# Kernel optimization log

Hardware: AMD Instinct MI355X
Metric: run time of the kernel (lower is better)

## Reference

```python
import jax, jax.numpy as jnp
import numpy as np

B, T_Q, T_KV, D = 4, 2048, 4096, 1024
H = 16
HD = D // H  # head_dim = 64
EPS_LN = 1e-5
EPS_NORM = 1e-12


def setup_inputs() -> dict:
    key = jax.random.key(0)
    ks = jax.random.split(key, 12)
    inp = {
        'query': jax.random.normal(ks[0], (B, T_Q, D), jnp.float32),
        'key':   jax.random.normal(ks[1], (B, T_KV, D), jnp.float32),
        'value': jax.random.normal(ks[2], (B, T_KV, D), jnp.float32),
        # projections (nn.Linear stores weight as [out, in]; y = x @ W.T)
        'Wq': jax.random.normal(ks[3], (D, D), jnp.float32) * 0.02,
        'Wk': jax.random.normal(ks[4], (D, D), jnp.float32) * 0.02,
        'Wv': jax.random.normal(ks[5], (D, D), jnp.float32) * 0.02,
        'Wo': jax.random.normal(ks[6], (D, D), jnp.float32) * 0.01,
        'bo': jnp.zeros((D,), jnp.float32),
        'Wbeta':  jax.random.normal(ks[7], (H, D), jnp.float32) * 0.02,
        'bbeta':  jnp.zeros((H,), jnp.float32),
        'Walpha': jax.random.normal(ks[8], (H, D), jnp.float32) * 0.02,
        'balpha': jnp.full((H,), -1.0, jnp.float32),
        # per-head-dim LayerNorms
        'gq': jnp.ones((HD,), jnp.float32),
        'bq': jnp.zeros((HD,), jnp.float32),
        'gk': jnp.ones((HD,), jnp.float32),
        'bk': jnp.zeros((HD,), jnp.float32),
    }
    return inp


def _layernorm(x, g, b):
    mu = jnp.mean(x, axis=-1, keepdims=True)
    var = jnp.mean(jnp.square(x - mu), axis=-1, keepdims=True)
    return (x - mu) * jax.lax.rsqrt(var + EPS_LN) * g + b


def reference(query, key, value, Wq, Wk, Wv, Wo, bo,
              Wbeta, bbeta, Walpha, balpha, gq, bq, gk, bk):
    Bq, Tq, Dm = query.shape
    Tkv = key.shape[1]

    q = (query @ Wq.T).reshape(Bq, Tq, H, HD)
    k = (key   @ Wk.T).reshape(Bq, Tkv, H, HD)
    v = (value @ Wv.T).reshape(Bq, Tkv, H, HD)

    q = _layernorm(q, gq, bq)
    k = _layernorm(k, gk, bk)
    # F.normalize(k, dim=-1)
    k = k / jnp.maximum(jnp.linalg.norm(k, axis=-1, keepdims=True), EPS_NORM)

    beta  = jax.nn.sigmoid(key @ Wbeta.T  + bbeta)   # [B, Tkv, H]
    alpha = jax.nn.sigmoid(key @ Walpha.T + balpha)  # [B, Tkv, H]

    # time-major for scan: [Tkv, B, H, ...]
    k_t = jnp.moveaxis(k, 1, 0)
    v_t = jnp.moveaxis(v, 1, 0)
    b_t = jnp.moveaxis(beta, 1, 0)
    a_t = jnp.moveaxis(alpha, 1, 0)

    M0 = jnp.zeros((Bq, H, HD, HD), query.dtype)

    def step(M, inputs):
        kt, vt, bt, at = inputs  # [B,H,d],[B,H,d],[B,H],[B,H]
        Mk = jnp.einsum('bhij,bhj->bhi', M, kt)
        erase = at[..., None, None] * jnp.einsum('bhi,bhj->bhij', Mk, kt)
        write = bt[..., None, None] * jnp.einsum('bhi,bhj->bhij', vt, kt)
        return M - erase + write, None

    M, _ = jax.lax.scan(step, M0, (k_t, v_t, b_t, a_t))

    # out[b,t,h,i] = sum_j M[b,h,i,j] * q[b,t,h,j]
    out = jnp.einsum('bhij,bthj->bthi', M, q).reshape(Bq, Tq, Dm)
    out = out @ Wo.T + bo  # dropout is identity in eval mode
    return out
```

## Files before the change

### kernel.cpp

```cpp
#include <hip/hip_runtime.h>
#include <math.h>

#define TQ_LEN 2048
#define TKV_LEN 4096
#define BATCH 4
#define DMODEL 1024
#define NH 16
#define HD 64
#define NKBA 1152
#define CCH 128
#define NCHUNK (TKV_LEN / CCH)

typedef unsigned short u16;
typedef __attribute__((ext_vector_type(8))) short bf16x8;
typedef __attribute__((ext_vector_type(4))) float f32x4;

__device__ __forceinline__ u16 f2bf(float x) {
  union { float f; unsigned u; } c; c.f = x;
  unsigned r = c.u + 0x7fffu + ((c.u >> 16) & 1u);
  return (u16)(r >> 16);
}
__device__ __forceinline__ float bf2f(u16 x) {
  union { unsigned u; float f; } c; c.u = ((unsigned)x) << 16;
  return c.f;
}

__device__ __forceinline__ float wave_sum64(float x) {
#pragma unroll
  for (int off = 32; off; off >>= 1) x += __shfl_xor(x, off, 64);
  return x;
}

__global__ __launch_bounds__(256) void cvt_bf16_kernel(
    const float* __restrict__ s, u16* __restrict__ d) {
  size_t i = ((size_t)blockIdx.x * 256 + threadIdx.x) * 8;
  float4 a = *(const float4*)&s[i];
  float4 b = *(const float4*)&s[i + 4];
  union { u16 h[8]; uint4 v; } o;
  o.h[0] = f2bf(a.x); o.h[1] = f2bf(a.y); o.h[2] = f2bf(a.z); o.h[3] = f2bf(a.w);
  o.h[4] = f2bf(b.x); o.h[5] = f2bf(b.y); o.h[6] = f2bf(b.z); o.h[7] = f2bf(b.w);
  *(uint4*)&d[i] = o.v;
}

__global__ __launch_bounds__(256) void wcat_bf_kernel(
    const float* __restrict__ Wk, const float* __restrict__ Wb,
    const float* __restrict__ Wa, u16* __restrict__ Wcat) {
  int i = blockIdx.x * 256 + threadIdx.x;
  int row = i / DMODEL, col = i % DMODEL;
  float v;
  if (row < 1024)      v = Wk[i];
  else if (row < 1040) v = Wb[(row - 1024) * DMODEL + col];
  else if (row < 1056) v = Wa[(row - 1040) * DMODEL + col];
  else                 v = 0.f;
  Wcat[i] = f2bf(v);
}

__device__ __forceinline__ void stage_tile_bf16(
    const u16* __restrict__ G, int ldg, int row0, int kcol0,
    u16* lds, int wid, int lane) {
#pragma unroll
  for (int e = 0; e < 2; ++e) {
    int r = (wid * 2 + e) * 16;
    const u16* g = G + (size_t)(row0 + r + (lane >> 2)) * ldg + kcol0 + (lane & 3) * 8;
    __builtin_amdgcn_global_load_lds(
        (const __attribute__((address_space(1))) void*)g,
        (__attribute__((address_space(3))) void*)(lds + r * 32), 16, 0, 0);
  }
}

template <bool HAS_BIAS, bool OUT_BF16>
__global__ __launch_bounds__(256) void gemm_bt_bf16(
    const u16* __restrict__ A, const u16* __restrict__ B,
    const float* __restrict__ bias, void* __restrict__ Cv,
    int M, int N, int K, int ldc, int nbx) {
  __shared__ u16 Al[2][128 * 32];
  __shared__ u16 Bl[2][128 * 32];
  const int tid = threadIdx.x;
  const int wid = tid >> 6, lane = tid & 63;
  const int wr = wid >> 1, wc = wid & 1;
  const int nwg = gridDim.x;
  const int cpx = nwg >> 3;
  const int orig = blockIdx.x;
  const int swz = (orig & 7) * cpx + (orig >> 3);
  const int bm = (swz / nbx) * 128, bn = (swz % nbx) * 128;
  const int lrow = lane & 15, lk = (lane >> 4) * 8;

  int aoff[4], boff[4];
#pragma unroll
  for (int f = 0; f < 4; ++f) {
    aoff[f] = (wr * 64 + f * 16 + lrow) * 32 + lk;
    boff[f] = (wc * 64 + f * 16 + lrow) * 32 + lk;
  }

  f32x4 acc[4][4] = {};
  const int nk = K >> 5;
  int cur = 0;
  stage_tile_bf16(A, K, bm, 0, &Al[0][0], wid, lane);
  stage_tile_bf16(B, K, bn, 0, &Bl[0][0], wid, lane);
  __syncthreads();
  for (int kt = 0; kt < nk; ++kt) {
    if (kt + 1 < nk) {
      stage_tile_bf16(A, K, bm, (kt + 1) * 32, &Al[cur ^ 1][0], wid, lane);
      stage_tile_bf16(B, K, bn, (kt + 1) * 32, &Bl[cur ^ 1][0], wid, lane);
    }
    bf16x8 af[4], bfr[4];
#pragma unroll
    for (int f = 0; f < 4; ++f) af[f] = *(const bf16x8*)&Al[cur][aoff[f]];
#pragma unroll
    for (int f = 0; f < 4; ++f) bfr[f] = *(const bf16x8*)&Bl[cur][boff[f]];
#pragma unroll
    for (int mf = 0; mf < 4; ++mf)
#pragma unroll
      for (int nf = 0; nf < 4; ++nf)
        acc[mf][nf] = __builtin_amdgcn_mfma_f32_16x16x32_bf16(
            af[mf], bfr[nf], acc[mf][nf], 0, 0, 0);
    __syncthreads();
    cur ^= 1;
  }
  const int crow0 = bm + wr * 64 + (lane >> 4) * 4;
  const int ccol0 = bn + wc * 64 + (lane & 15);
#pragma unroll
  for (int mf = 0; mf < 4; ++mf)
#pragma unroll
    for (int nf = 0; nf < 4; ++nf) {
      int col = ccol0 + nf * 16;
      float bv = HAS_BIAS ? bias[col] : 0.f;
#pragma unroll
      for (int i = 0; i < 4; ++i) {
        int row = crow0 + mf * 16 + i;
        float vout = acc[mf][nf][i] + bv;
        if (OUT_BF16)
          ((u16*)Cv)[(size_t)row * ldc + col] = f2bf(vout);
        else
          ((float*)Cv)[(size_t)row * ldc + col] = vout;
      }
    }
}

__global__ __launch_bounds__(256) void ln_q_kernel(float* __restrict__ q,
                                                   const float* __restrict__ g,
                                                   const float* __restrict__ b) {
  int gidx = blockIdx.x * 4 + (threadIdx.x >> 6);
  int lane = threadIdx.x & 63;
  int row = gidx >> 4, h = gidx & 15;
  float* p = q + (size_t)row * DMODEL + h * HD + lane;
  float x = *p;
  float mu = wave_sum64(x) * (1.f / 64.f);
  float d = x - mu;
  float var = wave_sum64(d * d) * (1.f / 64.f);
  float y = d * rsqrtf(var + 1e-5f) * g[lane] + b[lane];
  *p = y;
}

__global__ __launch_bounds__(256) void ln_k_kernel(float* __restrict__ kb,
                                                   const float* __restrict__ g,
                                                   const float* __restrict__ b) {
  int gidx = blockIdx.x * 4 + (threadIdx.x >> 6);
  int lane = threadIdx.x & 63;
  int row = gidx >> 4, h = gidx & 15;
  float* p = kb + (size_t)row * NKBA + h * HD + lane;
  float x = *p;
  float mu = wave_sum64(x) * (1.f / 64.f);
  float d = x - mu;
  float var = wave_sum64(d * d) * (1.f / 64.f);
  float y = d * rsqrtf(var + 1e-5f) * g[lane] + b[lane];
  float s2 = wave_sum64(y * y);
  y = y / fmaxf(sqrtf(s2), 1e-12f);
  *p = y;
}

__global__ __launch_bounds__(256) void sig_kernel(
    const float* __restrict__ kb, const float* __restrict__ bb,
    const float* __restrict__ ba, float* __restrict__ beta,
    float* __restrict__ alpha) {
  int i = blockIdx.x * 256 + threadIdx.x;
  int row = i >> 4, h = i & 15;
  float lb = kb[(size_t)row * NKBA + 1024 + h] + bb[h];
  float la = kb[(size_t)row * NKBA + 1040 + h] + ba[h];
  beta[i]  = 1.f / (1.f + expf(-lb));
  alpha[i] = 1.f / (1.f + expf(-la));
}

__global__ __launch_bounds__(64, 2) void chunk_scan_kernel(
    const float* __restrict__ kb, const u16* __restrict__ v,
    const float* __restrict__ beta, const float* __restrict__ alpha,
    float* __restrict__ Pbuf, float* __restrict__ Sbuf) {
  __shared__ float klds[2][64];
  int slot = blockIdx.x;
  int bh = slot / NCHUNK, ck = slot % NCHUNK;
  int b = bh >> 4, h = bh & 15;
  int lane = threadIdx.x;
  int t0 = ck * CCH;
  const float* kbase = kb + ((size_t)b * TKV_LEN + t0) * NKBA + h * HD;
  const u16* vbase = v + ((size_t)b * TKV_LEN + t0) * DMODEL + h * HD;
  const float* bbase = beta + ((size_t)b * TKV_LEN + t0) * NH + h;
  const float* abase = alpha + ((size_t)b * TKV_LEN + t0) * NH + h;

  float P[64], S[64];
#pragma unroll
  for (int j = 0; j < 64; ++j) { P[j] = (j == lane) ? 1.f : 0.f; S[j] = 0.f; }

  klds[0][lane] = kbase[lane];
  float kn = kbase[(size_t)NKBA + lane];
  float vn = bf2f(vbase[lane]);
  float btn = bbase[0];
  float atn = abase[0];

  for (int t = 0; t < CCH; ++t) {
    float vc = vn, bt = btn, at = atn;
    if (t + 1 < CCH) {
      vn = bf2f(vbase[(size_t)(t + 1) * DMODEL + lane]);
      btn = bbase[(size_t)(t + 1) * NH];
      atn = abase[(size_t)(t + 1) * NH];
    }
    klds[(t + 1) & 1][lane] = kn;
    kn = (t + 2 < CCH) ? kbase[(size_t)(t + 2) * NKBA + lane] : 0.f;
    const float* kcur = klds[t & 1];
    float pk0 = 0.f, pk1 = 0.f, sk0 = 0.f, sk1 = 0.f;
#pragma unroll
    for (int g = 0; g < 4; ++g) {
      float4 ka = *(const float4*)&kcur[g * 16 + 0];
      float4 kc = *(const float4*)&kcur[g * 16 + 4];
      float4 ke = *(const float4*)&kcur[g * 16 + 8];
      float4 kg = *(const float4*)&kcur[g * 16 + 12];
      pk0 = fmaf(P[g*16+ 0], ka.x, pk0); pk1 = fmaf(P[g*16+ 1], ka.y, pk1);
      pk0 = fmaf(P[g*16+ 2], ka.z, pk0); pk1 = fmaf(P[g*16+ 3], ka.w, pk1);
      pk0 = fmaf(P[g*16+ 4], kc.x, pk0); pk1 = fmaf(P[g*16+ 5], kc.y, pk1);
      pk0 = fmaf(P[g*16+ 6], kc.z, pk0); pk1 = fmaf(P[g*16+ 7], kc.w, pk1);
      pk0 = fmaf(P[g*16+ 8], ke.x, pk0); pk1 = fmaf(P[g*16+ 9], ke.y, pk1);
      pk0 = fmaf(P[g*16+10], ke.z, pk0); pk1 = fmaf(P[g*16+11], ke.w, pk1);
      pk0 = fmaf(P[g*16+12], kg.x, pk0); pk1 = fmaf(P[g*16+13], kg.y, pk1);
      pk0 = fmaf(P[g*16+14], kg.z, pk0); pk1 = fmaf(P[g*16+15], kg.w, pk1);
      sk0 = fmaf(S[g*16+ 0], ka.x, sk0); sk1 = fmaf(S[g*16+ 1], ka.y, sk1);
      sk0 = fmaf(S[g*16+ 2], ka.z, sk0); sk1 = fmaf(S[g*16+ 3], ka.w, sk1);
      sk0 = fmaf(S[g*16+ 4], kc.x, sk0); sk1 = fmaf(S[g*16+ 5], kc.y, sk1);
      sk0 = fmaf(S[g*16+ 6], kc.z, sk0); sk1 = fmaf(S[g*16+ 7], kc.w, sk1);
      sk0 = fmaf(S[g*16+ 8], ke.x, sk0); sk1 = fmaf(S[g*16+ 9], ke.y, sk1);
      sk0 = fmaf(S[g*16+10], ke.z, sk0); sk1 = fmaf(S[g*16+11], ke.w, sk1);
      sk0 = fmaf(S[g*16+12], kg.x, sk0); sk1 = fmaf(S[g*16+13], kg.y, sk1);
      sk0 = fmaf(S[g*16+14], kg.z, sk0); sk1 = fmaf(S[g*16+15], kg.w, sk1);
    }
    float cp = -at * (pk0 + pk1);
    float cs = fmaf(bt, vc, -at * (sk0 + sk1));
#pragma unroll
    for (int g = 0; g < 4; ++g) {
      float4 ka = *(const float4*)&kcur[g * 16 + 0];
      float4 kc = *(const float4*)&kcur[g * 16 + 4];
      float4 ke = *(const float4*)&kcur[g * 16 + 8];
      float4 kg = *(const float4*)&kcur[g * 16 + 12];
      P[g*16+ 0] = fmaf(cp, ka.x, P[g*16+ 0]); P[g*16+ 1] = fmaf(cp, ka.y, P[g*16+ 1]);
      P[g*16+ 2] = fmaf(cp, ka.z, P[g*16+ 2]); P[g*16+ 3] = fmaf(cp, ka.w, P[g*16+ 3]);
      P[g*16+ 4] = fmaf(cp, kc.x, P[g*16+ 4]); P[g*16+ 5] = fmaf(cp, kc.y, P[g*16+ 5]);
      P[g*16+ 6] = fmaf(cp, kc.z, P[g*16+ 6]); P[g*16+ 7] = fmaf(cp, kc.w, P[g*16+ 7]);
      P[g*16+ 8] = fmaf(cp, ke.x, P[g*16+ 8]); P[g*16+ 9] = fmaf(cp, ke.y, P[g*16+ 9]);
      P[g*16+10] = fmaf(cp, ke.z, P[g*16+10]); P[g*16+11] = fmaf(cp, ke.w, P[g*16+11]);
      P[g*16+12] = fmaf(cp, kg.x, P[g*16+12]); P[g*16+13] = fmaf(cp, kg.y, P[g*16+13]);
      P[g*16+14] = fmaf(cp, kg.z, P[g*16+14]); P[g*16+15] = fmaf(cp, kg.w, P[g*16+15]);
      S[g*16+ 0] = fmaf(cs, ka.x, S[g*16+ 0]); S[g*16+ 1] = fmaf(cs, ka.y, S[g*16+ 1]);
      S[g*16+ 2] = fmaf(cs, ka.z, S[g*16+ 2]); S[g*16+ 3] = fmaf(cs, ka.w, S[g*16+ 3]);
      S[g*16+ 4] = fmaf(cs, kc.x, S[g*16+ 4]); S[g*16+ 5] = fmaf(cs, kc.y, S[g*16+ 5]);
      S[g*16+ 6] = fmaf(cs, kc.z, S[g*16+ 6]); S[g*16+ 7] = fmaf(cs, kc.w, S[g*16+ 7]);
      S[g*16+ 8] = fmaf(cs, ke.x, S[g*16+ 8]); S[g*16+ 9] = fmaf(cs, ke.y, S[g*16+ 9]);
      S[g*16+10] = fmaf(cs, ke.z, S[g*16+10]); S[g*16+11] = fmaf(cs, ke.w, S[g*16+11]);
      S[g*16+12] = fmaf(cs, kg.x, S[g*16+12]); S[g*16+13] = fmaf(cs, kg.y, S[g*16+13]);
      S[g*16+14] = fmaf(cs, kg.z, S[g*16+14]); S[g*16+15] = fmaf(cs, kg.w, S[g*16+15]);
    }
  }
  float* po = Pbuf + (size_t)slot * 4096 + (size_t)lane * 64;
  float* so = Sbuf + (size_t)slot * 4096 + (size_t)lane * 64;
#pragma unroll
  for (int j4 = 0; j4 < 16; ++j4) {
    *(float4*)&po[j4 * 4] = make_float4(P[4 * j4], P[4 * j4 + 1], P[4 * j4 + 2], P[4 * j4 + 3]);
    *(float4*)&so[j4 * 4] = make_float4(S[4 * j4], S[4 * j4 + 1], S[4 * j4 + 2], S[4 * j4 + 3]);
  }
}

__global__ __launch_bounds__(256) void fold_kernel(
    const float* __restrict__ Pin, const float* __restrict__ Sin,
    float* __restrict__ Pout, float* __restrict__ Sout, int nitems) {
  __shared__ float Pa[64][68], Sa[64][68], Pc[64][68], Sc[64][68];
  const int tid = threadIdx.x;
  const int r0 = (tid >> 4) * 4, c0 = (tid & 15) * 4;
  for (int l = tid; l < 4096; l += 256) {
    int r = l >> 6, c = l & 63;
    Pa[r][c] = (r == c) ? 1.f : 0.f;
    Sa[r][c] = 0.f;
  }
  for (int item = 0; item < nitems; ++item) {
    const float* pg = Pin + ((size_t)blockIdx.x * nitems + item) * 4096;
    const float* sg = Sin + ((size_t)blockIdx.x * nitems + item) * 4096;
#pragma unroll
    for (int e = 0; e < 4; ++e) {
      int l = tid * 16 + e * 4;
      int r = l >> 6, c = l & 63;
      *(float4*)&Pc[r][c] = *(const float4*)&pg[l];
      *(float4*)&Sc[r][c] = *(const float4*)&sg[l];
    }
    __syncthreads();
    float accP[4][4] = {}, accS[4][4] = {};
#pragma unroll 4
    for (int j4 = 0; j4 < 16; ++j4) {
      float bmat[4][4];
#pragma unroll
      for (int jj = 0; jj < 4; ++jj) {
        float4 t = *(const float4*)&Pc[j4 * 4 + jj][c0];
        bmat[jj][0] = t.x; bmat[jj][1] = t.y; bmat[jj][2] = t.z; bmat[jj][3] = t.w;
      }
#pragma unroll
      for (int rr = 0; rr < 4; ++rr) {
        float4 tp = *(const float4*)&Pa[r0 + rr][j4 * 4];
        float4 ts = *(const float4*)&Sa[r0 + rr][j4 * 4];
        float ap[4] = {tp.x, tp.y, tp.z, tp.w};
        float as[4] = {ts.x, ts.y, ts.z, ts.w};
#pragma unroll
        for (int jj = 0; jj < 4; ++jj)
#pragma unroll
          for (int cc = 0; cc < 4; ++cc) {
            accP[rr][cc] = fmaf(ap[jj], bmat[jj][cc], accP[rr][cc]);
            accS[rr][cc] = fmaf(as[jj], bmat[jj][cc], accS[rr][cc]);
          }
      }
    }
#pragma unroll
    for (int rr = 0; rr < 4; ++rr)
#pragma unroll
      for (int cc = 0; cc < 4; ++cc) accS[rr][cc] += Sc[r0 + rr][c0 + cc];
    __syncthreads();
#pragma unroll
    for (int rr = 0; rr < 4; ++rr)
#pragma unroll
      for (int cc = 0; cc < 4; ++cc) {
        Pa[r0 + rr][c0 + cc] = accP[rr][cc];
        Sa[r0 + rr][c0 + cc] = accS[rr][cc];
      }
  }
  __syncthreads();
  float* po = Pout + (size_t)blockIdx.x * 4096;
  float* so = Sout + (size_t)blockIdx.x * 4096;
#pragma unroll
  for (int e = 0; e < 4; ++e) {
    int l = tid * 16 + e * 4;
    int r = l >> 6, c = l & 63;
    *(float4*)&po[l] = *(const float4*)&Pa[r][c];
    *(float4*)&so[l] = *(const float4*)&Sa[r][c];
  }
}

__global__ __launch_bounds__(256) void outm_kernel(
    const float* __restrict__ Mg, const float* __restrict__ q,
    u16* __restrict__ attn) {
  __shared__ float Ml[64][65];
  int bh = blockIdx.x;
  int tchunk = blockIdx.y;
  int b = bh >> 4, h = bh & 15;
  int tid = threadIdx.x;
  const float* mg = Mg + (size_t)bh * 4096;
#pragma unroll
  for (int e = 0; e < 16; ++e) {
    int l = tid + e * 256;
    Ml[l >> 6][l & 63] = mg[l];
  }
  __syncthreads();
  int lane = tid & 63, tt = tid >> 6;
  const float* qb = q + ((size_t)b * TQ_LEN + tchunk * 256) * DMODEL + h * HD;
  u16* ob = attn + ((size_t)b * TQ_LEN + tchunk * 256) * DMODEL + h * HD;
  for (int it = 0; it < 64; ++it) {
    int t = it * 4 + tt;
    const float* qr = qb + (size_t)t * DMODEL;
    float acc = 0.f;
#pragma unroll
    for (int j4 = 0; j4 < 16; ++j4) {
      float4 qv = *(const float4*)&qr[j4 * 4];
      acc += Ml[lane][j4 * 4 + 0] * qv.x + Ml[lane][j4 * 4 + 1] * qv.y +
             Ml[lane][j4 * 4 + 2] * qv.z + Ml[lane][j4 * 4 + 3] * qv.w;
    }
    ob[(size_t)t * DMODEL + lane] = f2bf(acc);
  }
}

extern "C" void kernel_launch(void* const* d_in, const int* in_sizes, int n_in,
                              void* d_out, int out_size, void* d_ws,
                              size_t ws_size, hipStream_t stream) {
  const float* query = (const float*)d_in[0];
  const float* key   = (const float*)d_in[1];
  const float* value = (const float*)d_in[2];
  const float* Wq    = (const float*)d_in[3];
  const float* Wk    = (const float*)d_in[4];
  const float* Wv    = (const float*)d_in[5];
  const float* Wo    = (const float*)d_in[6];
  const float* bo    = (const float*)d_in[7];
  const float* Wbeta = (const float*)d_in[8];
  const float* bbeta = (const float*)d_in[9];
  const float* Walpha= (const float*)d_in[10];
  const float* balpha= (const float*)d_in[11];
  const float* gq    = (const float*)d_in[12];
  const float* bq    = (const float*)d_in[13];
  const float* gk    = (const float*)d_in[14];
  const float* bk    = (const float*)d_in[15];
  float* out = (float*)d_out;

  const int MQ = BATCH * TQ_LEN;
  const int MKV = BATCH * TKV_LEN;
  const int NSLOT = 64 * NCHUNK;

  float* ws = (float*)d_ws;
  size_t off = 0;
  u16* Wcat_bf = (u16*)(ws + off); off += (size_t)NKBA * DMODEL / 2;
  u16* Wq_bf   = (u16*)(ws + off); off += (size_t)DMODEL * DMODEL / 2;
  u16* Wv_bf   = (u16*)(ws + off); off += (size_t)DMODEL * DMODEL / 2;
  u16* Wo_bf   = (u16*)(ws + off); off += (size_t)DMODEL * DMODEL / 2;
  u16* qbf = (u16*)(ws + off); size_t qbf_f = off; off += (size_t)MQ * DMODEL / 2;
  u16* kbf = (u16*)(ws + off); size_t kbf_f = off; off += (size_t)MKV * DMODEL / 2;
  u16* vbf = (u16*)(ws + off); size_t vbf_f = off; off += (size_t)MKV * DMODEL / 2;
  float* qp   = ws + off; off += (size_t)MQ * DMODEL;
  float* kba  = ws + off; size_t kba_f = off; off += (size_t)MKV * NKBA;
  u16* vpb = (u16*)(ws + off); off += (size_t)MKV * DMODEL / 2;
  float* Pbuf = ws + kbf_f;
  float* Sbuf = ws + vbf_f;
  float* Gp   = ws + qbf_f;
  float* Gs   = ws + qbf_f + 1048576;
  float* Fp   = ws + qbf_f + 2097152;
  float* beta = ws + qbf_f + 2359296;
  float* alpha= ws + qbf_f + 2621440;
  float* Mg   = ws + qbf_f + 2883584;
  u16* attn_bf = (u16*)(ws + kba_f);

  wcat_bf_kernel<<<NKBA * DMODEL / 256, 256, 0, stream>>>(Wk, Wbeta, Walpha, Wcat_bf);
  cvt_bf16_kernel<<<DMODEL * DMODEL / 2048, 256, 0, stream>>>(Wq, Wq_bf);
  cvt_bf16_kernel<<<DMODEL * DMODEL / 2048, 256, 0, stream>>>(Wv, Wv_bf);
  cvt_bf16_kernel<<<DMODEL * DMODEL / 2048, 256, 0, stream>>>(Wo, Wo_bf);
  cvt_bf16_kernel<<<MQ * DMODEL / 2048, 256, 0, stream>>>(query, qbf);
  cvt_bf16_kernel<<<MKV * DMODEL / 2048, 256, 0, stream>>>(key, kbf);
  cvt_bf16_kernel<<<MKV * DMODEL / 2048, 256, 0, stream>>>(value, vbf);
  gemm_bt_bf16<false, false><<<(DMODEL / 128) * (MQ / 128), 256, 0, stream>>>(
      qbf, Wq_bf, nullptr, qp, MQ, DMODEL, DMODEL, DMODEL, DMODEL / 128);
  gemm_bt_bf16<false, false><<<(NKBA / 128) * (MKV / 128), 256, 0, stream>>>(
      kbf, Wcat_bf, nullptr, kba, MKV, NKBA, DMODEL, NKBA, NKBA / 128);
  gemm_bt_bf16<false, true><<<(DMODEL / 128) * (MKV / 128), 256, 0, stream>>>(
      vbf, Wv_bf, nullptr, vpb, MKV, DMODEL, DMODEL, DMODEL, DMODEL / 128);
  ln_q_kernel<<<MQ * NH / 4, 256, 0, stream>>>(qp, gq, bq);
  ln_k_kernel<<<MKV * NH / 4, 256, 0, stream>>>(kba, gk, bk);
  sig_kernel<<<MKV * NH / 256, 256, 0, stream>>>(kba, bbeta, balpha, beta, alpha);
  chunk_scan_kernel<<<NSLOT, 64, 0, stream>>>(kba, vpb, beta, alpha, Pbuf, Sbuf);
  fold_kernel<<<NSLOT / 8, 256, 0, stream>>>(Pbuf, Sbuf, Gp, Gs, 8);
  fold_kernel<<<64, 256, 0, stream>>>(Gp, Gs, Fp, Mg, 4);
  outm_kernel<<<dim3(64, TQ_LEN / 256), 256, 0, stream>>>(Mg, qp, attn_bf);
  gemm_bt_bf16<true, false><<<(DMODEL / 128) * (MQ / 128), 256, 0, stream>>>(
      attn_bf, Wo_bf, bo, out, MQ, DMODEL, DMODEL, DMODEL, DMODEL / 128);
  (void)in_sizes; (void)n_in; (void)out_size; (void)ws_size;
}
```

Before: 584.2 us.

## Co-schedule Q projection GEMM with chunk scan in one heterogeneous launch

Merges the Q projection GEMM and the per-chunk delta-rule scan into a single kernel: the first blocks run scan work with four waves each, and the remaining blocks run the 128x128 MFMA GEMM tile for Q. The aim is to fill idle compute units during the latency-bound scan with independent GEMM work, removing one serialized launch. Beta and alpha move to fresh workspace so they do not alias buffers the fused kernel writes, and ln_q runs after the fused kernel. The scan blocks now pack four waves under launch_bounds 256, which changes register and occupancy behaviour of the register-heavy scan and may cause spilling or lower occupancy.

```diff
diff --git a/kernel.cpp b/kernel.cpp
--- a/kernel.cpp
+++ b/kernel.cpp
@@ -137,6 +137,165 @@
     }
 }
 
+__global__ __launch_bounds__(256) void fused_qgemm_scan_kernel(
+    const u16* __restrict__ qbf, const u16* __restrict__ Wq_bf,
+    float* __restrict__ qp,
+    const float* __restrict__ kb, const u16* __restrict__ v,
+    const float* __restrict__ beta, const float* __restrict__ alpha,
+    float* __restrict__ Pbuf, float* __restrict__ Sbuf, int nscan) {
+  __shared__ u16 Al[2][128 * 32];
+  __shared__ u16 Bl[2][128 * 32];
+  __shared__ float klds[4][2][64];
+
+  if ((int)blockIdx.x >= nscan) {
+    const int tid = threadIdx.x;
+    const int wid = tid >> 6, lane = tid & 63;
+    const int wr = wid >> 1, wc = wid & 1;
+    const int nwg = gridDim.x - nscan;
+    const int cpx = nwg >> 3;
+    const int orig = (int)blockIdx.x - nscan;
+    const int swz = (orig & 7) * cpx + (orig >> 3);
+    const int nbx = DMODEL / 128;
+    const int bm = (swz / nbx) * 128, bn = (swz % nbx) * 128;
+    const int lrow = lane & 15, lk = (lane >> 4) * 8;
+
+    int aoff[4], boff[4];
+#pragma unroll
+    for (int f = 0; f < 4; ++f) {
+      aoff[f] = (wr * 64 + f * 16 + lrow) * 32 + lk;
+      boff[f] = (wc * 64 + f * 16 + lrow) * 32 + lk;
+    }
+
+    f32x4 acc[4][4] = {};
+    const int nk = DMODEL >> 5;
+    int cur = 0;
+    stage_tile_bf16(qbf, DMODEL, bm, 0, &Al[0][0], wid, lane);
+    stage_tile_bf16(Wq_bf, DMODEL, bn, 0, &Bl[0][0], wid, lane);
+    __syncthreads();
+    for (int kt = 0; kt < nk; ++kt) {
+      if (kt + 1 < nk) {
+        stage_tile_bf16(qbf, DMODEL, bm, (kt + 1) * 32, &Al[cur ^ 1][0], wid, lane);
+        stage_tile_bf16(Wq_bf, DMODEL, bn, (kt + 1) * 32, &Bl[cur ^ 1][0], wid, lane);
+      }
+      bf16x8 af[4], bfr[4];
+#pragma unroll
+      for (int f = 0; f < 4; ++f) af[f] = *(const bf16x8*)&Al[cur][aoff[f]];
+#pragma unroll
+      for (int f = 0; f < 4; ++f) bfr[f] = *(const bf16x8*)&Bl[cur][boff[f]];
+#pragma unroll
+      for (int mf = 0; mf < 4; ++mf)
+#pragma unroll
+        for (int nf = 0; nf < 4; ++nf)
+          acc[mf][nf] = __builtin_amdgcn_mfma_f32_16x16x32_bf16(
+              af[mf], bfr[nf], acc[mf][nf], 0, 0, 0);
+      __syncthreads();
+      cur ^= 1;
+    }
+    const int crow0 = bm + wr * 64 + (lane >> 4) * 4;
+    const int ccol0 = bn + wc * 64 + (lane & 15);
+#pragma unroll
+    for (int mf = 0; mf < 4; ++mf)
+#pragma unroll
+      for (int nf = 0; nf < 4; ++nf) {
+        int col = ccol0 + nf * 16;
+#pragma unroll
+        for (int i = 0; i < 4; ++i) {
+          int row = crow0 + mf * 16 + i;
+          qp[(size_t)row * DMODEL + col] = acc[mf][nf][i];
+        }
+      }
+  } else {
+    int wid = threadIdx.x >> 6;
+    int lane = threadIdx.x & 63;
+    int slot = (int)blockIdx.x * 4 + wid;
+    int bh = slot / NCHUNK, ck = slot % NCHUNK;
+    int b = bh >> 4, h = bh & 15;
+    int t0 = ck * CCH;
+    const float* kbase = kb + ((size_t)b * TKV_LEN + t0) * NKBA + h * HD;
+    const u16* vbase = v + ((size_t)b * TKV_LEN + t0) * DMODEL + h * HD;
+    const float* bbase = beta + ((size_t)b * TKV_LEN + t0) * NH + h;
+    const float* abase = alpha + ((size_t)b * TKV_LEN + t0) * NH + h;
+
+    float P[64], S[64];
+#pragma unroll
+    for (int j = 0; j < 64; ++j) { P[j] = (j == lane) ? 1.f : 0.f; S[j] = 0.f; }
+
+    klds[wid][0][lane] = kbase[lane];
+    float kn = kbase[(size_t)NKBA + lane];
+    float vn = bf2f(vbase[lane]);
+    float btn = bbase[0];
+    float atn = abase[0];
+
+    for (int t = 0; t < CCH; ++t) {
+      float vc = vn, bt = btn, at = atn;
+      if (t + 1 < CCH) {
+        vn = bf2f(vbase[(size_t)(t + 1) * DMODEL + lane]);
+        btn = bbase[(size_t)(t + 1) * NH];
+        atn = abase[(size_t)(t + 1) * NH];
+      }
+      klds[wid][(t + 1) & 1][lane] = kn;
+      kn = (t + 2 < CCH) ? kbase[(size_t)(t + 2) * NKBA + lane] : 0.f;
+      const float* kcur = klds[wid][t & 1];
+      float pk0 = 0.f, pk1 = 0.f, sk0 = 0.f, sk1 = 0.f;
+#pragma unroll
+      for (int g = 0; g < 4; ++g) {
+        float4 ka = *(const float4*)&kcur[g * 16 + 0];
+        float4 kc = *(const float4*)&kcur[g * 16 + 4];
+        float4 ke = *(const float4*)&kcur[g * 16 + 8];
+        float4 kg = *(const float4*)&kcur[g * 16 + 12];
+        pk0 = fmaf(P[g*16+ 0], ka.x, pk0); pk1 = fmaf(P[g*16+ 1], ka.y, pk1);
+        pk0 = fmaf(P[g*16+ 2], ka.z, pk0); pk1 = fmaf(P[g*16+ 3], ka.w, pk1);
+        pk0 = fmaf(P[g*16+ 4], kc.x, pk0); pk1 = fmaf(P[g*16+ 5], kc.y, pk1);
+        pk0 = fmaf(P[g*16+ 6], kc.z, pk0); pk1 = fmaf(P[g*16+ 7], kc.w, pk1);
+        pk0 = fmaf(P[g*16+ 8], ke.x, pk0); pk1 = fmaf(P[g*16+ 9], ke.y, pk1);
+        pk0 = fmaf(P[g*16+10], ke.z, pk0); pk1 = fmaf(P[g*16+11], ke.w, pk1);
+        pk0 = fmaf(P[g*16+12], kg.x, pk0); pk1 = fmaf(P[g*16+13], kg.y, pk1);
+        pk0 = fmaf(P[g*16+14], kg.z, pk0); pk1 = fmaf(P[g*16+15], kg.w, pk1);
+        sk0 = fmaf(S[g*16+ 0], ka.x, sk0); sk1 = fmaf(S[g*16+ 1], ka.y, sk1);
+        sk0 = fmaf(S[g*16+ 2], ka.z, sk0); sk1 = fmaf(S[g*16+ 3], ka.w, sk1);
+        sk0 = fmaf(S[g*16+ 4], kc.x, sk0); sk1 = fmaf(S[g*16+ 5], kc.y, sk1);
+        sk0 = fmaf(S[g*16+ 6], kc.z, sk0); sk1 = fmaf(S[g*16+ 7], kc.w, sk1);
+        sk0 = fmaf(S[g*16+ 8], ke.x, sk0); sk1 = fmaf(S[g*16+ 9], ke.y, sk1);
+        sk0 = fmaf(S[g*16+10], ke.z, sk0); sk1 = fmaf(S[g*16+11], ke.w, sk1);
+        sk0 = fmaf(S[g*16+12], kg.x, sk0); sk1 = fmaf(S[g*16+13], kg.y, sk1);
+        sk0 = fmaf(S[g*16+14], kg.z, sk0); sk1 = fmaf(S[g*16+15], kg.w, sk1);
+      }
+      float cp = -at * (pk0 + pk1);
+      float cs = fmaf(bt, vc, -at * (sk0 + sk1));
+#pragma unroll
+      for (int g = 0; g < 4; ++g) {
+        float4 ka = *(const float4*)&kcur[g * 16 + 0];
+        float4 kc = *(const float4*)&kcur[g * 16 + 4];
+        float4 ke = *(const float4*)&kcur[g * 16 + 8];
+        float4 kg = *(const float4*)&kcur[g * 16 + 12];
+        P[g*16+ 0] = fmaf(cp, ka.x, P[g*16+ 0]); P[g*16+ 1] = fmaf(cp, ka.y, P[g*16+ 1]);
+        P[g*16+ 2] = fmaf(cp, ka.z, P[g*16+ 2]); P[g*16+ 3] = fmaf(cp, ka.w, P[g*16+ 3]);
+        P[g*16+ 4] = fmaf(cp, kc.x, P[g*16+ 4]); P[g*16+ 5] = fmaf(cp, kc.y, P[g*16+ 5]);
+        P[g*16+ 6] = fmaf(cp, kc.z, P[g*16+ 6]); P[g*16+ 7] = fmaf(cp, kc.w, P[g*16+ 7]);
+        P[g*16+ 8] = fmaf(cp, ke.x, P[g*16+ 8]); P[g*16+ 9] = fmaf(cp, ke.y, P[g*16+ 9]);
+        P[g*16+10] = fmaf(cp, ke.z, P[g*16+10]); P[g*16+11] = fmaf(cp, ke.w, P[g*16+11]);
+        P[g*16+12] = fmaf(cp, kg.x, P[g*16+12]); P[g*16+13] = fmaf(cp, kg.y, P[g*16+13]);
+        P[g*16+14] = fmaf(cp, kg.z, P[g*16+14]); P[g*16+15] = fmaf(cp, kg.w, P[g*16+15]);
+        S[g*16+ 0] = fmaf(cs, ka.x, S[g*16+ 0]); S[g*16+ 1] = fmaf(cs, ka.y, S[g*16+ 1]);
+        S[g*16+ 2] = fmaf(cs, ka.z, S[g*16+ 2]); S[g*16+ 3] = fmaf(cs, ka.w, S[g*16+ 3]);
+        S[g*16+ 4] = fmaf(cs, kc.x, S[g*16+ 4]); S[g*16+ 5] = fmaf(cs, kc.y, S[g*16+ 5]);
+        S[g*16+ 6] = fmaf(cs, kc.z, S[g*16+ 6]); S[g*16+ 7] = fmaf(cs, kc.w, S[g*16+ 7]);
+        S[g*16+ 8] = fmaf(cs, ke.x, S[g*16+ 8]); S[g*16+ 9] = fmaf(cs, ke.y, S[g*16+ 9]);
+        S[g*16+10] = fmaf(cs, ke.z, S[g*16+10]); S[g*16+11] = fmaf(cs, ke.w, S[g*16+11]);
+        S[g*16+12] = fmaf(cs, kg.x, S[g*16+12]); S[g*16+13] = fmaf(cs, kg.y, S[g*16+13]);
+        S[g*16+14] = fmaf(cs, kg.z, S[g*16+14]); S[g*16+15] = fmaf(cs, kg.w, S[g*16+15]);
+      }
+    }
+    float* po = Pbuf + (size_t)slot * 4096 + (size_t)lane * 64;
+    float* so = Sbuf + (size_t)slot * 4096 + (size_t)lane * 64;
+#pragma unroll
+    for (int j4 = 0; j4 < 16; ++j4) {
+      *(float4*)&po[j4 * 4] = make_float4(P[4 * j4], P[4 * j4 + 1], P[4 * j4 + 2], P[4 * j4 + 3]);
+      *(float4*)&so[j4 * 4] = make_float4(S[4 * j4], S[4 * j4 + 1], S[4 * j4 + 2], S[4 * j4 + 3]);
+    }
+  }
+}
+
 __global__ __launch_bounds__(256) void ln_q_kernel(float* __restrict__ q,
                                                    const float* __restrict__ g,
                                                    const float* __restrict__ b) {
@@ -179,100 +338,6 @@
   float la = kb[(size_t)row * NKBA + 1040 + h] + ba[h];
   beta[i]  = 1.f / (1.f + expf(-lb));
   alpha[i] = 1.f / (1.f + expf(-la));
-}
-
-__global__ __launch_bounds__(64, 2) void chunk_scan_kernel(
-    const float* __restrict__ kb, const u16* __restrict__ v,
-    const float* __restrict__ beta, const float* __restrict__ alpha,
-    float* __restrict__ Pbuf, float* __restrict__ Sbuf) {
-  __shared__ float klds[2][64];
-  int slot = blockIdx.x;
-  int bh = slot / NCHUNK, ck = slot % NCHUNK;
-  int b = bh >> 4, h = bh & 15;
-  int lane = threadIdx.x;
-  int t0 = ck * CCH;
-  const float* kbase = kb + ((size_t)b * TKV_LEN + t0) * NKBA + h * HD;
-  const u16* vbase = v + ((size_t)b * TKV_LEN + t0) * DMODEL + h * HD;
-  const float* bbase = beta + ((size_t)b * TKV_LEN + t0) * NH + h;
-  const float* abase = alpha + ((size_t)b * TKV_LEN + t0) * NH + h;
-
-  float P[64], S[64];
-#pragma unroll
-  for (int j = 0; j < 64; ++j) { P[j] = (j == lane) ? 1.f : 0.f; S[j] = 0.f; }
-
-  klds[0][lane] = kbase[lane];
-  float kn = kbase[(size_t)NKBA + lane];
-  float vn = bf2f(vbase[lane]);
-  float btn = bbase[0];
-  float atn = abase[0];
-
-  for (int t = 0; t < CCH; ++t) {
-    float vc = vn, bt = btn, at = atn;
-    if (t + 1 < CCH) {
-      vn = bf2f(vbase[(size_t)(t + 1) * DMODEL + lane]);
-      btn = bbase[(size_t)(t + 1) * NH];
-      atn = abase[(size_t)(t + 1) * NH];
-    }
-    klds[(t + 1) & 1][lane] = kn;
-    kn = (t + 2 < CCH) ? kbase[(size_t)(t + 2) * NKBA + lane] : 0.f;
-    const float* kcur = klds[t & 1];
-    float pk0 = 0.f, pk1 = 0.f, sk0 = 0.f, sk1 = 0.f;
-#pragma unroll
-    for (int g = 0; g < 4; ++g) {
-      float4 ka = *(const float4*)&kcur[g * 16 + 0];
-      float4 kc = *(const float4*)&kcur[g * 16 + 4];
-      float4 ke = *(const float4*)&kcur[g * 16 + 8];
-      float4 kg = *(const float4*)&kcur[g * 16 + 12];
-      pk0 = fmaf(P[g*16+ 0], ka.x, pk0); pk1 = fmaf(P[g*16+ 1], ka.y, pk1);
-      pk0 = fmaf(P[g*16+ 2], ka.z, pk0); pk1 = fmaf(P[g*16+ 3], ka.w, pk1);
-      pk0 = fmaf(P[g*16+ 4], kc.x, pk0); pk1 = fmaf(P[g*16+ 5], kc.y, pk1);
-      pk0 = fmaf(P[g*16+ 6], kc.z, pk0); pk1 = fmaf(P[g*16+ 7], kc.w, pk1);
-      pk0 = fmaf(P[g*16+ 8], ke.x, pk0); pk1 = fmaf(P[g*16+ 9], ke.y, pk1);
-      pk0 = fmaf(P[g*16+10], ke.z, pk0); pk1 = fmaf(P[g*16+11], ke.w, pk1);
-      pk0 = fmaf(P[g*16+12], kg.x, pk0); pk1 = fmaf(P[g*16+13], kg.y, pk1);
-      pk0 = fmaf(P[g*16+14], kg.z, pk0); pk1 = fmaf(P[g*16+15], kg.w, pk1);
-      sk0 = fmaf(S[g*16+ 0], ka.x, sk0); sk1 = fmaf(S[g*16+ 1], ka.y, sk1);
-      sk0 = fmaf(S[g*16+ 2], ka.z, sk0); sk1 = fmaf(S[g*16+ 3], ka.w, sk1);
-      sk0 = fmaf(S[g*16+ 4], kc.x, sk0); sk1 = fmaf(S[g*16+ 5], kc.y, sk1);
-      sk0 = fmaf(S[g*16+ 6], kc.z, sk0); sk1 = fmaf(S[g*16+ 7], kc.w, sk1);
-      sk0 = fmaf(S[g*16+ 8], ke.x, sk0); sk1 = fmaf(S[g*16+ 9], ke.y, sk1);
-      sk0 = fmaf(S[g*16+10], ke.z, sk0); sk1 = fmaf(S[g*16+11], ke.w, sk1);
-      sk0 = fmaf(S[g*16+12], kg.x, sk0); sk1 = fmaf(S[g*16+13], kg.y, sk1);
-      sk0 = fmaf(S[g*16+14], kg.z, sk0); sk1 = fmaf(S[g*16+15], kg.w, sk1);
-    }
-    float cp = -at * (pk0 + pk1);
-    float cs = fmaf(bt, vc, -at * (sk0 + sk1));
-#pragma unroll
-    for (int g = 0; g < 4; ++g) {
-      float4 ka = *(const float4*)&kcur[g * 16 + 0];
-      float4 kc = *(const float4*)&kcur[g * 16 + 4];
-      float4 ke = *(const float4*)&kcur[g * 16 + 8];
-      float4 kg = *(const float4*)&kcur[g * 16 + 12];
-      P[g*16+ 0] = fmaf(cp, ka.x, P[g*16+ 0]); P[g*16+ 1] = fmaf(cp, ka.y, P[g*16+ 1]);
-      P[g*16+ 2] = fmaf(cp, ka.z, P[g*16+ 2]); P[g*16+ 3] = fmaf(cp, ka.w, P[g*16+ 3]);
-      P[g*16+ 4] = fmaf(cp, kc.x, P[g*16+ 4]); P[g*16+ 5] = fmaf(cp, kc.y, P[g*16+ 5]);
-      P[g*16+ 6] = fmaf(cp, kc.z, P[g*16+ 6]); P[g*16+ 7] = fmaf(cp, kc.w, P[g*16+ 7]);
-      P[g*16+ 8] = fmaf(cp, ke.x, P[g*16+ 8]); P[g*16+ 9] = fmaf(cp, ke.y, P[g*16+ 9]);
-      P[g*16+10] = fmaf(cp, ke.z, P[g*16+10]); P[g*16+11] = fmaf(cp, ke.w, P[g*16+11]);
-      P[g*16+12] = fmaf(cp, kg.x, P[g*16+12]); P[g*16+13] = fmaf(cp, kg.y, P[g*16+13]);
-      P[g*16+14] = fmaf(cp, kg.z, P[g*16+14]); P[g*16+15] = fmaf(cp, kg.w, P[g*16+15]);
-      S[g*16+ 0] = fmaf(cs, ka.x, S[g*16+ 0]); S[g*16+ 1] = fmaf(cs, ka.y, S[g*16+ 1]);
-      S[g*16+ 2] = fmaf(cs, ka.z, S[g*16+ 2]); S[g*16+ 3] = fmaf(cs, ka.w, S[g*16+ 3]);
-      S[g*16+ 4] = fmaf(cs, kc.x, S[g*16+ 4]); S[g*16+ 5] = fmaf(cs, kc.y, S[g*16+ 5]);
-      S[g*16+ 6] = fmaf(cs, kc.z, S[g*16+ 6]); S[g*16+ 7] = fmaf(cs, kc.w, S[g*16+ 7]);
-      S[g*16+ 8] = fmaf(cs, ke.x, S[g*16+ 8]); S[g*16+ 9] = fmaf(cs, ke.y, S[g*16+ 9]);
-      S[g*16+10] = fmaf(cs, ke.z, S[g*16+10]); S[g*16+11] = fmaf(cs, ke.w, S[g*16+11]);
-      S[g*16+12] = fmaf(cs, kg.x, S[g*16+12]); S[g*16+13] = fmaf(cs, kg.y, S[g*16+13]);
-      S[g*16+14] = fmaf(cs, kg.z, S[g*16+14]); S[g*16+15] = fmaf(cs, kg.w, S[g*16+15]);
-    }
-  }
-  float* po = Pbuf + (size_t)slot * 4096 + (size_t)lane * 64;
-  float* so = Sbuf + (size_t)slot * 4096 + (size_t)lane * 64;
-#pragma unroll
-  for (int j4 = 0; j4 < 16; ++j4) {
-    *(float4*)&po[j4 * 4] = make_float4(P[4 * j4], P[4 * j4 + 1], P[4 * j4 + 2], P[4 * j4 + 3]);
-    *(float4*)&so[j4 * 4] = make_float4(S[4 * j4], S[4 * j4 + 1], S[4 * j4 + 2], S[4 * j4 + 3]);
-  }
 }
 
 __global__ __launch_bounds__(256) void fold_kernel(
@@ -415,14 +480,14 @@
   float* qp   = ws + off; off += (size_t)MQ * DMODEL;
   float* kba  = ws + off; size_t kba_f = off; off += (size_t)MKV * NKBA;
   u16* vpb = (u16*)(ws + off); off += (size_t)MKV * DMODEL / 2;
+  float* beta = ws + off; off += (size_t)MKV * NH;
+  float* alpha= ws + off; off += (size_t)MKV * NH;
   float* Pbuf = ws + kbf_f;
   float* Sbuf = ws + vbf_f;
   float* Gp   = ws + qbf_f;
   float* Gs   = ws + qbf_f + 1048576;
   float* Fp   = ws + qbf_f + 2097152;
-  float* beta = ws + qbf_f + 2359296;
-  float* alpha= ws + qbf_f + 2621440;
-  float* Mg   = ws + qbf_f + 2883584;
+  float* Mg   = ws + qbf_f + 2359296;
   u16* attn_bf = (u16*)(ws + kba_f);
 
   wcat_bf_kernel<<<NKBA * DMODEL / 256, 256, 0, stream>>>(Wk, Wbeta, Walpha, Wcat_bf);
@@ -432,16 +497,16 @@
   cvt_bf16_kernel<<<MQ * DMODEL / 2048, 256, 0, stream>>>(query, qbf);
   cvt_bf16_kernel<<<MKV * DMODEL / 2048, 256, 0, stream>>>(key, kbf);
   cvt_bf16_kernel<<<MKV * DMODEL / 2048, 256, 0, stream>>>(value, vbf);
-  gemm_bt_bf16<false, false><<<(DMODEL / 128) * (MQ / 128), 256, 0, stream>>>(
-      qbf, Wq_bf, nullptr, qp, MQ, DMODEL, DMODEL, DMODEL, DMODEL / 128);
   gemm_bt_bf16<false, false><<<(NKBA / 128) * (MKV / 128), 256, 0, stream>>>(
       kbf, Wcat_bf, nullptr, kba, MKV, NKBA, DMODEL, NKBA, NKBA / 128);
   gemm_bt_bf16<false, true><<<(DMODEL / 128) * (MKV / 128), 256, 0, stream>>>(
       vbf, Wv_bf, nullptr, vpb, MKV, DMODEL, DMODEL, DMODEL, DMODEL / 128);
-  ln_q_kernel<<<MQ * NH / 4, 256, 0, stream>>>(qp, gq, bq);
   ln_k_kernel<<<MKV * NH / 4, 256, 0, stream>>>(kba, gk, bk);
   sig_kernel<<<MKV * NH / 256, 256, 0, stream>>>(kba, bbeta, balpha, beta, alpha);
-  chunk_scan_kernel<<<NSLOT, 64, 0, stream>>>(kba, vpb, beta, alpha, Pbuf, Sbuf);
+  fused_qgemm_scan_kernel<<<NSLOT / 4 + (DMODEL / 128) * (MQ / 128), 256, 0,
+                            stream>>>(qbf, Wq_bf, qp, kba, vpb, beta, alpha,
+                                      Pbuf, Sbuf, NSLOT / 4);
+  ln_q_kernel<<<MQ * NH / 4, 256, 0, stream>>>(qp, gq, bq);
   fold_kernel<<<NSLOT / 8, 256, 0, stream>>>(Pbuf, Sbuf, Gp, Gs, 8);
   fold_kernel<<<64, 256, 0, stream>>>(Gp, Gs, Fp, Mg, 4);
   outm_kernel<<<dim3(64, TQ_LEN / 256), 256, 0, stream>>>(Mg, qp, attn_bf);
```

Result: slower. 675.1 us (+15.6%).
